# Optimization experiments

Measured on AMD Instinct MI355X. Metric: run time of the kernel, lower is better.

The kernel has to match this reference:

```python
import jax, jax.numpy as jnp
import numpy as np

NUM_STEPS = 16
FD_EPS = 1e-4  # finite-difference step used by the torch TraceEstimator


def setup_inputs() -> dict:
    key = jax.random.key(0)
    ks = jax.random.split(key, 8)
    B, D, H = 65536, 64, 256
    x = jax.random.normal(ks[0], (B, D), dtype=jnp.float32)
    eps = jax.random.normal(ks[1], (NUM_STEPS, B, D), dtype=jnp.float32)
    W0 = jax.random.normal(ks[2], (D + 1, H), dtype=jnp.float32) / np.sqrt(D + 1)
    b0 = jnp.zeros((H,), dtype=jnp.float32)
    W1 = jax.random.normal(ks[3], (H, H), dtype=jnp.float32) / np.sqrt(H)
    b1 = jnp.zeros((H,), dtype=jnp.float32)
    W2 = jax.random.normal(ks[4], (H, D), dtype=jnp.float32) / np.sqrt(H)
    b2 = jnp.zeros((D,), dtype=jnp.float32)
    return {"x": x, "eps": eps, "W0": W0, "b0": b0, "W1": W1, "b1": b1, "W2": W2, "b2": b2}


def _dynamics(t, x, W0, b0, W1, b1, W2, b2):
    # concat scalar time as an extra feature column, 2-hidden-layer ReLU MLP, residual
    tcol = jnp.full((x.shape[0], 1), t, dtype=x.dtype)
    h = jnp.concatenate([x, tcol], axis=-1)          # [B, D+1]
    h = jax.nn.relu(h @ W0 + b0)                     # [B, H]
    h = jax.nn.relu(h @ W1 + b1)                     # [B, H]
    return x + (h @ W2 + b2)                         # residual, [B, D]


def reference(x, eps, W0, b0, W1, b1, W2, b2):
    dt = 1.0 / NUM_STEPS
    f = lambda t, xx: _dynamics(t, xx, W0, b0, W1, b1, W2, b2)

    def step(carry, inputs):
        xc, ld = carry
        t, e = inputs
        # Hutchinson trace via finite-difference JVP (matches torch TraceEstimator)
        base = f(t, xc)                               # also serves as RK4 k1
        plus = f(t, xc + 0.5 * e * FD_EPS)
        jvp = (plus - base) / FD_EPS
        trace = jnp.sum(e * jvp, axis=-1)             # [B]
        ld = ld - trace * dt
        # RK4 step
        k1 = base
        k2 = f(t + dt / 2, xc + dt * k1 / 2)
        k3 = f(t + dt / 2, xc + dt * k2 / 2)
        k4 = f(t + dt, xc + dt * k3)
        xn = xc + dt * (k1 + 2 * k2 + 2 * k3 + k4) / 6
        return (xn, ld), None

    ts = jnp.arange(NUM_STEPS, dtype=x.dtype) * dt
    log_det0 = jnp.zeros((x.shape[0],), dtype=x.dtype)
    (x_out, log_det), _ = jax.lax.scan(step, (x, log_det0), (ts, eps))
    return x_out, log_det
```

## Files before the change

### kernel.cpp

```cpp
#include <hip/hip_runtime.h>

#define NSTEP 16
#define BATCH 65536
#define DD 64
#define HH 256
#define MT 64
#define H0S 264
#define ABSTR 72

typedef _Float16 half8 __attribute__((ext_vector_type(8)));
typedef float floatx4 __attribute__((ext_vector_type(4)));

__global__ __launch_bounds__(256) void prep_weights(
    const float* __restrict__ W0, const float* __restrict__ W1,
    const float* __restrict__ W2, _Float16* __restrict__ ws)
{
    int i = blockIdx.x * 256 + threadIdx.x;
    _Float16* Wt0 = ws;
    _Float16* Wt1 = ws + 16384;
    _Float16* Wt2 = ws + 16384 + 65536;
    { int n = i >> 8, k = i & 255; Wt1[i] = (_Float16)W1[k * HH + n]; }
    if (i < 16384) {
        { int n = i >> 6, k = i & 63;  Wt0[i] = (_Float16)W0[k * HH + n]; }
        { int n = i >> 8, k = i & 255; Wt2[i] = (_Float16)W2[k * DD + n]; }
    }
}

template<bool MASKED>
__device__ __forceinline__ void mlp_pass(
    const _Float16* __restrict__ Wt0, const _Float16* __restrict__ Wt1,
    const _Float16* __restrict__ Wt2,
    const float* __restrict__ b1g, const float* __restrict__ b2g,
    _Float16* h0, _Float16* h1, const _Float16* ab, const float* c0buf,
    int wave, int quad, int l16, float* outv)
{
    const floatx4 zero4 = {0.f, 0.f, 0.f, 0.f};

    floatx4 acc[4][4];
#pragma unroll
    for (int rt = 0; rt < 4; rt++)
#pragma unroll
        for (int ct = 0; ct < 4; ct++) acc[rt][ct] = zero4;
#pragma unroll
    for (int kc = 0; kc < 2; kc++) {
        half8 af[4], bf[4];
#pragma unroll
        for (int rt = 0; rt < 4; rt++)
            af[rt] = *(const half8*)(ab + (rt * 16 + l16) * ABSTR + kc * 32 + quad * 8);
#pragma unroll
        for (int ct = 0; ct < 4; ct++)
            bf[ct] = *(const half8*)(Wt0 + (wave * 64 + ct * 16 + l16) * DD + kc * 32 + quad * 8);
#pragma unroll
        for (int rt = 0; rt < 4; rt++)
#pragma unroll
            for (int ct = 0; ct < 4; ct++)
                acc[rt][ct] = __builtin_amdgcn_mfma_f32_16x16x32_f16(af[rt], bf[ct], acc[rt][ct], 0, 0, 0);
    }
#pragma unroll
    for (int ct = 0; ct < 4; ct++) {
        int col = wave * 64 + ct * 16 + l16;
        float cb = MASKED ? 0.f : c0buf[col];
#pragma unroll
        for (int rt = 0; rt < 4; rt++)
#pragma unroll
            for (int rr = 0; rr < 4; rr++) {
                int row = rt * 16 + quad * 4 + rr;
                float v = acc[rt][ct][rr];
                if (MASKED) {
                    float z = (float)h0[row * H0S + col];
                    h0[row * H0S + col] = (_Float16)(z > 0.f ? v : 0.f);
                } else {
                    v += cb;
                    h0[row * H0S + col] = (_Float16)(v > 0.f ? v : 0.f);
                }
            }
    }
    __syncthreads();

#pragma unroll
    for (int rt = 0; rt < 4; rt++)
#pragma unroll
        for (int ct = 0; ct < 4; ct++) acc[rt][ct] = zero4;
#pragma unroll
    for (int kc = 0; kc < 8; kc++) {
        half8 af[4], bf[4];
#pragma unroll
        for (int rt = 0; rt < 4; rt++)
            af[rt] = *(const half8*)(h0 + (rt * 16 + l16) * H0S + kc * 32 + quad * 8);
#pragma unroll
        for (int ct = 0; ct < 4; ct++)
            bf[ct] = *(const half8*)(Wt1 + (wave * 64 + ct * 16 + l16) * HH + kc * 32 + quad * 8);
#pragma unroll
        for (int rt = 0; rt < 4; rt++)
#pragma unroll
            for (int ct = 0; ct < 4; ct++)
                acc[rt][ct] = __builtin_amdgcn_mfma_f32_16x16x32_f16(af[rt], bf[ct], acc[rt][ct], 0, 0, 0);
    }
#pragma unroll
    for (int ct = 0; ct < 4; ct++) {
        int col = wave * 64 + ct * 16 + l16;
        float cb = MASKED ? 0.f : b1g[col];
#pragma unroll
        for (int rt = 0; rt < 4; rt++)
#pragma unroll
            for (int rr = 0; rr < 4; rr++) {
                int row = rt * 16 + quad * 4 + rr;
                float v = acc[rt][ct][rr];
                if (MASKED) {
                    float z = (float)h1[row * H0S + col];
                    h1[row * H0S + col] = (_Float16)(z > 0.f ? v : 0.f);
                } else {
                    v += cb;
                    h1[row * H0S + col] = (_Float16)(v > 0.f ? v : 0.f);
                }
            }
    }
    __syncthreads();

    floatx4 a2[4];
#pragma unroll
    for (int rt = 0; rt < 4; rt++) a2[rt] = zero4;
#pragma unroll
    for (int kc = 0; kc < 8; kc++) {
        half8 bf2 = *(const half8*)(Wt2 + (wave * 16 + l16) * HH + kc * 32 + quad * 8);
#pragma unroll
        for (int rt = 0; rt < 4; rt++) {
            half8 af = *(const half8*)(h1 + (rt * 16 + l16) * H0S + kc * 32 + quad * 8);
            a2[rt] = __builtin_amdgcn_mfma_f32_16x16x32_f16(af, bf2, a2[rt], 0, 0, 0);
        }
    }
    float bb2 = MASKED ? 0.f : b2g[wave * 16 + l16];
#pragma unroll
    for (int rt = 0; rt < 4; rt++)
#pragma unroll
        for (int rr = 0; rr < 4; rr++) outv[rt * 4 + rr] = a2[rt][rr] + bb2;
}

__global__ __launch_bounds__(256, 2) void ffjord_kernel(
    const float* __restrict__ xg, const float* __restrict__ epsg,
    const float* __restrict__ W0g, const float* __restrict__ b0g,
    const float* __restrict__ b1g, const float* __restrict__ b2g,
    const _Float16* __restrict__ ws, float* __restrict__ out)
{
    __shared__ __attribute__((aligned(16))) _Float16 h0[MT * H0S];
    __shared__ __attribute__((aligned(16))) _Float16 h1[MT * H0S];
    __shared__ __attribute__((aligned(16))) _Float16 ab[MT * ABSTR];
    __shared__ float c0buf[HH];
    __shared__ float ldacc[MT];

    const _Float16* Wt0 = ws;
    const _Float16* Wt1 = ws + 16384;
    const _Float16* Wt2 = ws + 16384 + 65536;

    const int tid  = threadIdx.x;
    const int wave = tid >> 6;
    const int lane = tid & 63;
    const int quad = lane >> 4;
    const int l16  = lane & 15;
    const int row0 = blockIdx.x * MT;
    const int colD = wave * 16 + l16;
    const float dt = 1.f / NSTEP;

    if (tid < MT) ldacc[tid] = 0.f;

    float x[16];
#pragma unroll
    for (int i = 0; i < 16; i++) {
        int r = (i >> 2) * 16 + quad * 4 + (i & 3);
        x[i] = xg[(size_t)(row0 + r) * DD + colD];
    }

#pragma unroll 1
    for (int s = 0; s < NSTEP; s++) {
        float t = s * dt;
        float e[16];
#pragma unroll
        for (int i = 0; i < 16; i++) {
            int r = (i >> 2) * 16 + quad * 4 + (i & 3);
            e[i] = epsg[(size_t)(s * BATCH + row0 + r) * DD + colD];
        }
        float xacc[16], kprev[16], yv[16], outv[16];
#pragma unroll
        for (int i = 0; i < 16; i++) { xacc[i] = x[i]; kprev[i] = 0.f; }

#pragma unroll 1
        for (int p = 0; p < 5; p++) {
            if (p == 1) {
#pragma unroll
                for (int i = 0; i < 16; i++) yv[i] = 0.5f * e[i];
#pragma unroll
                for (int i = 0; i < 16; i++) {
                    int r = (i >> 2) * 16 + quad * 4 + (i & 3);
                    ab[r * ABSTR + colD] = (_Float16)yv[i];
                }
                __syncthreads();
                mlp_pass<true>(Wt0, Wt1, Wt2, b1g, b2g, h0, h1, ab, c0buf,
                               wave, quad, l16, outv);
#pragma unroll
                for (int i = 0; i < 16; i++) {
                    float pr = e[i] * (0.5f * e[i] + outv[i]);
                    pr += __shfl_xor(pr, 1);
                    pr += __shfl_xor(pr, 2);
                    pr += __shfl_xor(pr, 4);
                    pr += __shfl_xor(pr, 8);
                    if (l16 == 0) {
                        int r = (i >> 2) * 16 + quad * 4 + (i & 3);
                        atomicAdd(&ldacc[r], -dt * pr);
                    }
                }
            } else {
                float c  = (p == 4) ? 1.f : 0.5f;
                float w  = (p == 0 || p == 4) ? dt / 6.f : dt / 3.f;
                float tp = t + ((p == 4) ? dt : (p >= 2 ? 0.5f * dt : 0.f));
#pragma unroll
                for (int i = 0; i < 16; i++) yv[i] = x[i] + c * dt * kprev[i];
#pragma unroll
                for (int i = 0; i < 16; i++) {
                    int r = (i >> 2) * 16 + quad * 4 + (i & 3);
                    ab[r * ABSTR + colD] = (_Float16)yv[i];
                }
                c0buf[tid] = tp * W0g[64 * HH + tid] + b0g[tid];
                __syncthreads();
                mlp_pass<false>(Wt0, Wt1, Wt2, b1g, b2g, h0, h1, ab, c0buf,
                                wave, quad, l16, outv);
#pragma unroll
                for (int i = 0; i < 16; i++) {
                    kprev[i] = yv[i] + outv[i];
                    xacc[i] += w * kprev[i];
                }
            }
        }
#pragma unroll
        for (int i = 0; i < 16; i++) x[i] = xacc[i];
    }

#pragma unroll
    for (int i = 0; i < 16; i++) {
        int r = (i >> 2) * 16 + quad * 4 + (i & 3);
        out[(size_t)(row0 + r) * DD + colD] = x[i];
    }
    __syncthreads();
    if (tid < MT) out[(size_t)BATCH * DD + row0 + tid] = ldacc[tid];
}

extern "C" void kernel_launch(void* const* d_in, const int* in_sizes, int n_in,
                              void* d_out, int out_size, void* d_ws, size_t ws_size,
                              hipStream_t stream) {
    const float* xg   = (const float*)d_in[0];
    const float* epsg = (const float*)d_in[1];
    const float* W0g  = (const float*)d_in[2];
    const float* b0g  = (const float*)d_in[3];
    const float* W1g  = (const float*)d_in[4];
    const float* b1g  = (const float*)d_in[5];
    const float* W2g  = (const float*)d_in[6];
    const float* b2g  = (const float*)d_in[7];
    float* outp = (float*)d_out;
    _Float16* ws = (_Float16*)d_ws;

    prep_weights<<<65536 / 256, 256, 0, stream>>>(W0g, W1g, W2g, ws);
    ffjord_kernel<<<BATCH / MT, 256, 0, stream>>>(xg, epsg, W0g, b0g, b1g, b2g, ws, outp);
}
```

Measured before the change: 2.949 ms.

## Keep ReLU masks in registers, hoist biases, defer trace reduction to end

Records the ReLU activation masks from the base pass as 64-bit register bitmasks, so the masked finite-difference pass no longer reads h0/h1 back from LDS. Bias and time-weight loads are hoisted out of the step loop into registers. The per-step shuffle reduction and LDS atomics for the trace are replaced by per-lane register accumulation that is reduced once at the end. Eps loading moves into the trace pass, and the launch bounds are given as explicit waves-per-EU attributes. The extra mask and accumulator registers add pressure at a fixed two waves per EU and could cause spills.

```diff
diff --git a/kernel.cpp b/kernel.cpp
--- a/kernel.cpp
+++ b/kernel.cpp
@@ -26,13 +26,14 @@
     }
 }
 
-template<bool MASKED>
+template<int MODE>
 __device__ __forceinline__ void mlp_pass(
     const _Float16* __restrict__ Wt0, const _Float16* __restrict__ Wt1,
     const _Float16* __restrict__ Wt2,
-    const float* __restrict__ b1g, const float* __restrict__ b2g,
+    const float* b1v, float b2v,
     _Float16* h0, _Float16* h1, const _Float16* ab, const float* c0buf,
-    int wave, int quad, int l16, float* outv)
+    int wave, int quad, int l16, float* outv,
+    unsigned long long& m0, unsigned long long& m1)
 {
     const floatx4 zero4 = {0.f, 0.f, 0.f, 0.f};
 
@@ -56,24 +57,31 @@
             for (int ct = 0; ct < 4; ct++)
                 acc[rt][ct] = __builtin_amdgcn_mfma_f32_16x16x32_f16(af[rt], bf[ct], acc[rt][ct], 0, 0, 0);
     }
-#pragma unroll
-    for (int ct = 0; ct < 4; ct++) {
-        int col = wave * 64 + ct * 16 + l16;
-        float cb = MASKED ? 0.f : c0buf[col];
-#pragma unroll
-        for (int rt = 0; rt < 4; rt++)
-#pragma unroll
-            for (int rr = 0; rr < 4; rr++) {
-                int row = rt * 16 + quad * 4 + rr;
-                float v = acc[rt][ct][rr];
-                if (MASKED) {
-                    float z = (float)h0[row * H0S + col];
-                    h0[row * H0S + col] = (_Float16)(z > 0.f ? v : 0.f);
-                } else {
-                    v += cb;
-                    h0[row * H0S + col] = (_Float16)(v > 0.f ? v : 0.f);
-                }
-            }
+    {
+        unsigned long long mnew = 0;
+#pragma unroll
+        for (int ct = 0; ct < 4; ct++) {
+            int col = wave * 64 + ct * 16 + l16;
+            float cb = (MODE == 1) ? 0.f : c0buf[col];
+#pragma unroll
+            for (int rt = 0; rt < 4; rt++)
+#pragma unroll
+                for (int rr = 0; rr < 4; rr++) {
+                    int row = rt * 16 + quad * 4 + rr;
+                    int idx = (ct << 4) | (rt << 2) | rr;
+                    float v = acc[rt][ct][rr];
+                    bool pos;
+                    if (MODE == 1) {
+                        pos = (m0 >> idx) & 1ull;
+                    } else {
+                        v += cb;
+                        pos = v > 0.f;
+                        if (MODE == 0) mnew |= (unsigned long long)pos << idx;
+                    }
+                    h0[row * H0S + col] = pos ? (_Float16)v : (_Float16)0.f;
+                }
+        }
+        if (MODE == 0) m0 = mnew;
     }
     __syncthreads();
 
@@ -96,24 +104,31 @@
             for (int ct = 0; ct < 4; ct++)
                 acc[rt][ct] = __builtin_amdgcn_mfma_f32_16x16x32_f16(af[rt], bf[ct], acc[rt][ct], 0, 0, 0);
     }
-#pragma unroll
-    for (int ct = 0; ct < 4; ct++) {
-        int col = wave * 64 + ct * 16 + l16;
-        float cb = MASKED ? 0.f : b1g[col];
-#pragma unroll
-        for (int rt = 0; rt < 4; rt++)
-#pragma unroll
-            for (int rr = 0; rr < 4; rr++) {
-                int row = rt * 16 + quad * 4 + rr;
-                float v = acc[rt][ct][rr];
-                if (MASKED) {
-                    float z = (float)h1[row * H0S + col];
-                    h1[row * H0S + col] = (_Float16)(z > 0.f ? v : 0.f);
-                } else {
-                    v += cb;
-                    h1[row * H0S + col] = (_Float16)(v > 0.f ? v : 0.f);
-                }
-            }
+    {
+        unsigned long long mnew = 0;
+#pragma unroll
+        for (int ct = 0; ct < 4; ct++) {
+            float cb = (MODE == 1) ? 0.f : b1v[ct];
+            int col = wave * 64 + ct * 16 + l16;
+#pragma unroll
+            for (int rt = 0; rt < 4; rt++)
+#pragma unroll
+                for (int rr = 0; rr < 4; rr++) {
+                    int row = rt * 16 + quad * 4 + rr;
+                    int idx = (ct << 4) | (rt << 2) | rr;
+                    float v = acc[rt][ct][rr];
+                    bool pos;
+                    if (MODE == 1) {
+                        pos = (m1 >> idx) & 1ull;
+                    } else {
+                        v += cb;
+                        pos = v > 0.f;
+                        if (MODE == 0) mnew |= (unsigned long long)pos << idx;
+                    }
+                    h1[row * H0S + col] = pos ? (_Float16)v : (_Float16)0.f;
+                }
+        }
+        if (MODE == 0) m1 = mnew;
     }
     __syncthreads();
 
@@ -129,14 +144,15 @@
             a2[rt] = __builtin_amdgcn_mfma_f32_16x16x32_f16(af, bf2, a2[rt], 0, 0, 0);
         }
     }
-    float bb2 = MASKED ? 0.f : b2g[wave * 16 + l16];
+    float bb2 = (MODE == 1) ? 0.f : b2v;
 #pragma unroll
     for (int rt = 0; rt < 4; rt++)
 #pragma unroll
         for (int rr = 0; rr < 4; rr++) outv[rt * 4 + rr] = a2[rt][rr] + bb2;
 }
 
-__global__ __launch_bounds__(256, 2) void ffjord_kernel(
+__global__ __attribute__((amdgpu_flat_work_group_size(256, 256), amdgpu_waves_per_eu(2, 2)))
+void ffjord_kernel(
     const float* __restrict__ xg, const float* __restrict__ epsg,
     const float* __restrict__ W0g, const float* __restrict__ b0g,
     const float* __restrict__ b1g, const float* __restrict__ b2g,
@@ -161,6 +177,13 @@
     const int colD = wave * 16 + l16;
     const float dt = 1.f / NSTEP;
 
+    const float wtime = W0g[64 * HH + tid];
+    const float b0v   = b0g[tid];
+    float b1v[4];
+#pragma unroll
+    for (int ct = 0; ct < 4; ct++) b1v[ct] = b1g[wave * 64 + ct * 16 + l16];
+    const float b2v = b2g[wave * 16 + l16];
+
     if (tid < MT) ldacc[tid] = 0.f;
 
     float x[16];
@@ -169,49 +192,44 @@
         int r = (i >> 2) * 16 + quad * 4 + (i & 3);
         x[i] = xg[(size_t)(row0 + r) * DD + colD];
     }
+    float ldreg[16];
+#pragma unroll
+    for (int i = 0; i < 16; i++) ldreg[i] = 0.f;
+
+    unsigned long long m0 = 0, m1 = 0;
 
 #pragma unroll 1
     for (int s = 0; s < NSTEP; s++) {
         float t = s * dt;
-        float e[16];
-#pragma unroll
-        for (int i = 0; i < 16; i++) {
-            int r = (i >> 2) * 16 + quad * 4 + (i & 3);
-            e[i] = epsg[(size_t)(s * BATCH + row0 + r) * DD + colD];
-        }
-        float xacc[16], kprev[16], yv[16], outv[16];
+        float xacc[16], kprev[16], outv[16];
 #pragma unroll
         for (int i = 0; i < 16; i++) { xacc[i] = x[i]; kprev[i] = 0.f; }
 
 #pragma unroll 1
         for (int p = 0; p < 5; p++) {
             if (p == 1) {
-#pragma unroll
-                for (int i = 0; i < 16; i++) yv[i] = 0.5f * e[i];
+                float e[16];
 #pragma unroll
                 for (int i = 0; i < 16; i++) {
                     int r = (i >> 2) * 16 + quad * 4 + (i & 3);
-                    ab[r * ABSTR + colD] = (_Float16)yv[i];
+                    e[i] = epsg[(size_t)(s * BATCH + row0 + r) * DD + colD];
+                }
+#pragma unroll
+                for (int i = 0; i < 16; i++) {
+                    int r = (i >> 2) * 16 + quad * 4 + (i & 3);
+                    ab[r * ABSTR + colD] = (_Float16)(0.5f * e[i]);
                 }
                 __syncthreads();
-                mlp_pass<true>(Wt0, Wt1, Wt2, b1g, b2g, h0, h1, ab, c0buf,
-                               wave, quad, l16, outv);
-#pragma unroll
-                for (int i = 0; i < 16; i++) {
-                    float pr = e[i] * (0.5f * e[i] + outv[i]);
-                    pr += __shfl_xor(pr, 1);
-                    pr += __shfl_xor(pr, 2);
-                    pr += __shfl_xor(pr, 4);
-                    pr += __shfl_xor(pr, 8);
-                    if (l16 == 0) {
-                        int r = (i >> 2) * 16 + quad * 4 + (i & 3);
-                        atomicAdd(&ldacc[r], -dt * pr);
-                    }
-                }
+                mlp_pass<1>(Wt0, Wt1, Wt2, b1v, b2v, h0, h1, ab, c0buf,
+                            wave, quad, l16, outv, m0, m1);
+#pragma unroll
+                for (int i = 0; i < 16; i++)
+                    ldreg[i] -= dt * (e[i] * (0.5f * e[i] + outv[i]));
             } else {
                 float c  = (p == 4) ? 1.f : 0.5f;
                 float w  = (p == 0 || p == 4) ? dt / 6.f : dt / 3.f;
                 float tp = t + ((p == 4) ? dt : (p >= 2 ? 0.5f * dt : 0.f));
+                float yv[16];
 #pragma unroll
                 for (int i = 0; i < 16; i++) yv[i] = x[i] + c * dt * kprev[i];
 #pragma unroll
@@ -219,10 +237,14 @@
                     int r = (i >> 2) * 16 + quad * 4 + (i & 3);
                     ab[r * ABSTR + colD] = (_Float16)yv[i];
                 }
-                c0buf[tid] = tp * W0g[64 * HH + tid] + b0g[tid];
+                c0buf[tid] = tp * wtime + b0v;
                 __syncthreads();
-                mlp_pass<false>(Wt0, Wt1, Wt2, b1g, b2g, h0, h1, ab, c0buf,
-                                wave, quad, l16, outv);
+                if (p == 0)
+                    mlp_pass<0>(Wt0, Wt1, Wt2, b1v, b2v, h0, h1, ab, c0buf,
+                                wave, quad, l16, outv, m0, m1);
+                else
+                    mlp_pass<2>(Wt0, Wt1, Wt2, b1v, b2v, h0, h1, ab, c0buf,
+                                wave, quad, l16, outv, m0, m1);
 #pragma unroll
                 for (int i = 0; i < 16; i++) {
                     kprev[i] = yv[i] + outv[i];
@@ -238,6 +260,18 @@
     for (int i = 0; i < 16; i++) {
         int r = (i >> 2) * 16 + quad * 4 + (i & 3);
         out[(size_t)(row0 + r) * DD + colD] = x[i];
+    }
+#pragma unroll
+    for (int i = 0; i < 16; i++) {
+        float pr = ldreg[i];
+        pr += __shfl_xor(pr, 1);
+        pr += __shfl_xor(pr, 2);
+        pr += __shfl_xor(pr, 4);
+        pr += __shfl_xor(pr, 8);
+        if (l16 == 0) {
+            int r = (i >> 2) * 16 + quad * 4 + (i & 3);
+            atomicAdd(&ldacc[r], pr);
+        }
     }
     __syncthreads();
     if (tid < MT) out[(size_t)BATCH * DD + row0 + tid] = ldacc[tid];
```

New measurement: 3.565 ms. 20.9% more time.
